# Kernel optimization log

Measured on AMD Instinct MI355X. Metric: run time of the kernel, lower is better.

## Reference

```python
import jax, jax.numpy as jnp
import numpy as np

EMBED_DIM = 1024
NUM_HEADS = 16
HEAD_DIM = EMBED_DIM // NUM_HEADS
SCALE = HEAD_DIM ** -0.5


def setup_inputs() -> dict:
    key = jax.random.key(0)
    k_x, k_qkv, k_proj = jax.random.split(key, 3)
    x = jax.random.normal(k_x, (2, 2048, EMBED_DIM), dtype=jnp.float32)
    # nn.Linear weights: [out_features, in_features]
    w_qkv = jax.random.normal(k_qkv, (3 * EMBED_DIM, EMBED_DIM), dtype=jnp.float32) * (EMBED_DIM ** -0.5)
    w_proj = jax.random.normal(k_proj, (EMBED_DIM, EMBED_DIM), dtype=jnp.float32) * (EMBED_DIM ** -0.5)
    return {"x": x, "w_qkv": w_qkv, "w_proj": w_proj}


def reference(x, w_qkv, w_proj):
    B, N, C = x.shape
    # fused QKV projection: [B,N,3C]
    qkv = jnp.einsum('bnc,oc->bno', x, w_qkv)
    qkv = qkv.reshape(B, N, 3, NUM_HEADS, HEAD_DIM)
    q, k, v = jnp.moveaxis(qkv, 2, 0)  # each [B, N, H, D]
    q = q.transpose(0, 2, 1, 3)  # [B, H, N, D]
    k = k.transpose(0, 2, 1, 3)
    v = v.transpose(0, 2, 1, 3)
    # scaled dot-product attention (eval mode: dropout_p=0, non-causal)
    scores = jnp.einsum('bhqd,bhkd->bhqk', q, k) * SCALE
    attn = jax.nn.softmax(scores, axis=-1)
    out = jnp.einsum('bhqk,bhkd->bhqd', attn, v)  # [B, H, N, D]
    out = out.transpose(0, 2, 1, 3).reshape(B, N, C)
    return jnp.einsum('bnc,oc->bno', out, w_proj)
```

## Files before the change

### kernel.cpp

```cpp
#include <hip/hip_runtime.h>
#include <hip/hip_bf16.h>

typedef __bf16 bf16;
typedef __bf16 bf16x8 __attribute__((ext_vector_type(8)));
typedef __bf16 bf16x4 __attribute__((ext_vector_type(4)));
typedef _Float16 f16;
typedef _Float16 f16x4 __attribute__((ext_vector_type(4)));
typedef float f32x4 __attribute__((ext_vector_type(4)));

#define MFMA16(a, b, c)    __builtin_amdgcn_mfma_f32_16x16x32_bf16(a, b, c, 0, 0, 0)
#define MFMA16F16(a, b, c) __builtin_amdgcn_mfma_f32_16x16x16f16(a, b, c, 0, 0, 0)

__device__ __forceinline__ void gll(const void* g, void* l) {
    __builtin_amdgcn_global_load_lds(
        (const __attribute__((address_space(1))) unsigned int*)g,
        (__attribute__((address_space(3))) unsigned int*)l, 16, 0, 0);
}

__global__ void cvt_all(const float* __restrict__ x, const float* __restrict__ wq,
                        const float* __restrict__ wp, bf16* __restrict__ xb,
                        bf16* __restrict__ wqb, bf16* __restrict__ wpb) {
    int i = blockIdx.x * 256 + threadIdx.x;
    const float4* s; bf16* d; int j;
    if (i < 1048576)                { s = (const float4*)x;  d = xb;  j = i; }
    else if (i < 1048576 + 786432)  { s = (const float4*)wq; d = wqb; j = i - 1048576; }
    else                            { s = (const float4*)wp; d = wpb; j = i - 1835008; }
    float4 f = s[j];
    bf16x4 o; o[0] = (bf16)f.x; o[1] = (bf16)f.y; o[2] = (bf16)f.z; o[3] = (bf16)f.w;
    ((bf16x4*)d)[j] = o;
}

#define QSCALE 0.18033688f

__global__ __launch_bounds__(256, 3) void gemm_qkv(
    const bf16* __restrict__ A, const bf16* __restrict__ Bm,
    bf16* __restrict__ qo, bf16* __restrict__ ko, f16* __restrict__ vo)
{
    __shared__ bf16 As[2][128 * 32];
    __shared__ bf16 Bs[2][128 * 32];
    const int tid = threadIdx.x;
    const int wave = tid >> 6, lane = tid & 63;
    const int lrow = lane & 15, quad = lane >> 4;
    const int wm = (wave >> 1) * 64, wn = (wave & 1) * 64;
    const int srow = tid >> 2;
    const int scol = ((tid & 3) ^ (srow & 3)) * 8;
    const int fsw = (quad ^ (lrow & 3)) * 8;

    const bf16* Ap = A + (long)(blockIdx.x * 128 + srow) * 1024 + scol;
    const bf16* Bp = Bm + (long)(blockIdx.y * 128 + srow) * 1024 + scol;

    f32x4 acc[4][4] = {};
    const int gm0 = blockIdx.x * 128 + wm;
    const int go0 = blockIdx.y * 128 + wn;

    gll(Ap, &As[0][tid * 8]);  gll(Ap + 64 * 1024, &As[0][2048 + tid * 8]);
    gll(Bp, &Bs[0][tid * 8]);  gll(Bp + 64 * 1024, &Bs[0][2048 + tid * 8]);

    if (blockIdx.y < 16) {
        for (int i = 0; i < 32; i++) {
            const int cur = i & 1;
            __syncthreads();
            if (i < 31) {
                const int k0 = (i + 1) * 32;
                gll(Ap + k0, &As[cur ^ 1][tid * 8]);
                gll(Ap + 64 * 1024 + k0, &As[cur ^ 1][2048 + tid * 8]);
                gll(Bp + k0, &Bs[cur ^ 1][tid * 8]);
                gll(Bp + 64 * 1024 + k0, &Bs[cur ^ 1][2048 + tid * 8]);
            }
            bf16x8 af[4], bfr[4];
#pragma unroll
            for (int ii = 0; ii < 4; ii++) af[ii] = *(const bf16x8*)&As[cur][(wm + ii * 16 + lrow) * 32 + fsw];
#pragma unroll
            for (int j = 0; j < 4; j++) bfr[j] = *(const bf16x8*)&Bs[cur][(wn + j * 16 + lrow) * 32 + fsw];
#pragma unroll
            for (int ii = 0; ii < 4; ii++)
#pragma unroll
                for (int j = 0; j < 4; j++)
                    acc[ii][j] = MFMA16(bfr[j], af[ii], acc[ii][j]);
        }
        const bool isQ = blockIdx.y < 8;
        bf16* dst = isQ ? qo : ko;
        const float sc = isQ ? QSCALE : 1.0f;
#pragma unroll
        for (int i = 0; i < 4; i++) {
            int gm = gm0 + i * 16 + lrow;
            int b = gm >> 11, n = gm & 2047;
#pragma unroll
            for (int j = 0; j < 4; j++) {
                int ob = go0 + j * 16 + quad * 4;
                int rem = ob & 1023;
                int h = rem >> 6, d0 = rem & 63;
                bf16x4 pk;
#pragma unroll
                for (int r = 0; r < 4; r++) pk[r] = (bf16)(acc[i][j][r] * sc);
                *(bf16x4*)&dst[((long)(b * 16 + h) * 2048 + n) * 64 + d0] = pk;
            }
        }
    } else {
        for (int i = 0; i < 32; i++) {
            const int cur = i & 1;
            __syncthreads();
            if (i < 31) {
                const int k0 = (i + 1) * 32;
                gll(Ap + k0, &As[cur ^ 1][tid * 8]);
                gll(Ap + 64 * 1024 + k0, &As[cur ^ 1][2048 + tid * 8]);
                gll(Bp + k0, &Bs[cur ^ 1][tid * 8]);
                gll(Bp + 64 * 1024 + k0, &Bs[cur ^ 1][2048 + tid * 8]);
            }
            bf16x8 af[4], bfr[4];
#pragma unroll
            for (int ii = 0; ii < 4; ii++) af[ii] = *(const bf16x8*)&As[cur][(wm + ii * 16 + lrow) * 32 + fsw];
#pragma unroll
            for (int j = 0; j < 4; j++) bfr[j] = *(const bf16x8*)&Bs[cur][(wn + j * 16 + lrow) * 32 + fsw];
#pragma unroll
            for (int ii = 0; ii < 4; ii++)
#pragma unroll
                for (int j = 0; j < 4; j++)
                    acc[ii][j] = MFMA16(af[ii], bfr[j], acc[ii][j]);
        }
#pragma unroll
        for (int i = 0; i < 4; i++) {
            int gmb = gm0 + i * 16 + quad * 4;
            int b = gmb >> 11, nb = gmb & 2047;
#pragma unroll
            for (int j = 0; j < 4; j++) {
                int o = go0 + j * 16 + lrow;
                int rem = o & 1023;
                int h = rem >> 6, d = rem & 63;
                f16x4 pk;
#pragma unroll
                for (int r = 0; r < 4; r++) pk[r] = (f16)acc[i][j][r];
                *(f16x4*)&vo[(((long)(b * 16 + h)) * 64 + d) * 2048 + nb] = pk;
            }
        }
    }
}

__global__ __launch_bounds__(256, 2) void attn_kernel(
    const bf16* __restrict__ q, const bf16* __restrict__ k,
    const f16* __restrict__ vt, bf16* __restrict__ o)
{
    __shared__ __align__(16) char smem[35328];
    bf16* KsB = (bf16*)smem;

    const int tid = threadIdx.x, wave = tid >> 6, lane = tid & 63;
    const int lrow = lane & 15, quad = lane >> 4;
    const int qh = wave & 1, kh = wave >> 1;
    const int bh = blockIdx.x & 31, qt = blockIdx.x >> 5;
    const bf16* Qp = q + ((long)bh * 2048 + qt * 128 + qh * 64) * 64;
    const bf16* Kp = k + (long)bh * 2048 * 64;
    const f16*  Vp = vt + (long)bh * 64 * 2048;

    const int sr = tid >> 3;
    const int scc = ((tid & 7) ^ (sr & 7)) * 8;

    bf16x8 qf[4][2];
#pragma unroll
    for (int t = 0; t < 4; t++)
#pragma unroll
        for (int ks = 0; ks < 2; ks++)
            qf[t][ks] = *(const bf16x8*)&Qp[(t * 16 + lrow) * 64 + ks * 32 + quad * 8];
    asm volatile("s_waitcnt vmcnt(0)" ::: "memory");

#pragma unroll
    for (int b = 0; b < 2; b++) {
        gll(Kp + b * 4096 + sr * 64 + scc,        KsB + b * 4096 + tid * 8);
        gll(Kp + b * 4096 + (sr + 32) * 64 + scc, KsB + b * 4096 + 2048 + tid * 8);
    }

    f32x4 oacc[4][4] = {};
    float lsum[4] = {0.f, 0.f, 0.f, 0.f};

    for (int kv = 0; kv < 32; kv++) {
        asm volatile("s_waitcnt vmcnt(2)" ::: "memory");
        __builtin_amdgcn_s_barrier();
        asm volatile("" ::: "memory");

        f16x4 vfr[2][4];
#pragma unroll
        for (int n = 0; n < 2; n++)
#pragma unroll
            for (int jd = 0; jd < 4; jd++)
                vfr[n][jd] = *(const f16x4*)&Vp[(long)(jd * 16 + lrow) * 2048 +
                                                kv * 64 + kh * 32 + n * 16 + quad * 4];

        if (kv < 30) {
            bf16* kd = KsB + ((kv + 2) & 3) * 4096;
            gll(Kp + (kv + 2) * 4096 + sr * 64 + scc,        kd + tid * 8);
            gll(Kp + (kv + 2) * 4096 + (sr + 32) * 64 + scc, kd + 2048 + tid * 8);
        }

        const bf16* Kc = KsB + (kv & 3) * 4096;

        bf16x8 kf[2][2];
#pragma unroll
        for (int ks = 0; ks < 2; ks++)
#pragma unroll
            for (int n = 0; n < 2; n++)
                kf[ks][n] = *(const bf16x8*)&Kc[(kh * 32 + n * 16 + lrow) * 64 +
                                                (((ks * 4 + quad) ^ (lrow & 7)) * 8)];
        f32x4 sacc[4][2];
#pragma unroll
        for (int t = 0; t < 4; t++)
#pragma unroll
            for (int n = 0; n < 2; n++) sacc[t][n] = f32x4{-8.f, -8.f, -8.f, -8.f};
        __builtin_amdgcn_s_setprio(1);
#pragma unroll
        for (int ks = 0; ks < 2; ks++)
#pragma unroll
            for (int t = 0; t < 4; t++)
#pragma unroll
                for (int n = 0; n < 2; n++)
                    sacc[t][n] = MFMA16(kf[ks][n], qf[t][ks], sacc[t][n]);
        __builtin_amdgcn_s_setprio(0);

        f16x4 pa[4][2];
#pragma unroll
        for (int t = 0; t < 4; t++)
#pragma unroll
            for (int n = 0; n < 2; n++)
#pragma unroll
                for (int r = 0; r < 4; r++) {
                    float p = __builtin_exp2f(sacc[t][n][r]);
                    lsum[t] += p;
                    pa[t][n][r] = (f16)p;
                }

        __builtin_amdgcn_s_setprio(1);
#pragma unroll
        for (int jd = 0; jd < 4; jd++)
#pragma unroll
            for (int t = 0; t < 4; t++)
#pragma unroll
                for (int n = 0; n < 2; n++)
                    oacc[t][jd] = MFMA16F16(pa[t][n], vfr[n][jd], oacc[t][jd]);
        __builtin_amdgcn_s_setprio(0);
    }

#pragma unroll
    for (int t = 0; t < 4; t++) {
        lsum[t] += __shfl_xor(lsum[t], 16, 64);
        lsum[t] += __shfl_xor(lsum[t], 32, 64);
    }

    __syncthreads();
    float* Pt  = (float*)smem;
    float* lsL = (float*)(smem + 34816);
    float* Pr  = Pt + qh * (64 * 68);
    if (kh == 1) {
#pragma unroll
        for (int t = 0; t < 4; t++)
#pragma unroll
            for (int jd = 0; jd < 4; jd++)
                *(f32x4*)&Pr[lane * 68 + (t * 4 + jd) * 4] = oacc[t][jd];
        if (quad == 0)
#pragma unroll
            for (int t = 0; t < 4; t++) lsL[qh * 64 + t * 16 + lrow] = lsum[t];
    }
    __syncthreads();
    if (kh == 0) {
#pragma unroll
        for (int t = 0; t < 4; t++)
#pragma unroll
            for (int jd = 0; jd < 4; jd++)
                oacc[t][jd] += *(const f32x4*)&Pr[lane * 68 + (t * 4 + jd) * 4];
#pragma unroll
        for (int t = 0; t < 4; t++) lsum[t] += lsL[qh * 64 + t * 16 + lrow];

        bf16* Tw = (bf16*)Pr;
        const int b = bh >> 4, h = bh & 15;
#pragma unroll
        for (int t = 0; t < 4; t++) {
            float linv = 1.0f / lsum[t];
#pragma unroll
            for (int r = 0; r < 4; r++) {
                float lr = __shfl(linv, quad * 4 + r, 64);
#pragma unroll
                for (int jd = 0; jd < 4; jd++)
                    Tw[(t * 16 + quad * 4 + r) * 72 + jd * 16 + lrow] = (bf16)(oacc[t][jd][r] * lr);
            }
        }
        const int rr = lane >> 3, cc = (lane & 7) * 8;
#pragma unroll
        for (int p = 0; p < 8; p++) {
            bf16x8 val = *(const bf16x8*)&Tw[(rr + p * 8) * 72 + cc];
            int n = qt * 128 + qh * 64 + rr + p * 8;
            *(bf16x8*)&o[((long)(b * 2048 + n)) * 1024 + h * 64 + cc] = val;
        }
    }
}

__global__ __launch_bounds__(256, 2) void gemm_proj(
    const bf16* __restrict__ A, const bf16* __restrict__ Bm, float* __restrict__ out)
{
    __shared__ bf16 As[2][128 * 32];
    __shared__ bf16 Bs[2][64 * 32];
    const int tid = threadIdx.x;
    const int wave = tid >> 6, lane = tid & 63;
    const int lrow = lane & 15, quad = lane >> 4;
    const int wm = (wave >> 1) * 64, wn = (wave & 1) * 32;
    const int srow = tid >> 2;
    const int scol = ((tid & 3) ^ (srow & 3)) * 8;
    const int fsw = (quad ^ (lrow & 3)) * 8;

    const bf16* Ap = A + (long)(blockIdx.x * 128 + srow) * 1024 + scol;
    const bf16* Bp = Bm + (long)(blockIdx.y * 64 + srow) * 1024 + scol;

    f32x4 acc[4][2] = {};

    gll(Ap, &As[0][tid * 8]);  gll(Ap + 64 * 1024, &As[0][2048 + tid * 8]);
    gll(Bp, &Bs[0][tid * 8]);

    for (int i = 0; i < 32; i++) {
        const int cur = i & 1;
        __syncthreads();
        if (i < 31) {
            const int k0 = (i + 1) * 32;
            gll(Ap + k0, &As[cur ^ 1][tid * 8]);
            gll(Ap + 64 * 1024 + k0, &As[cur ^ 1][2048 + tid * 8]);
            gll(Bp + k0, &Bs[cur ^ 1][tid * 8]);
        }
        bf16x8 af[4], bfr[2];
#pragma unroll
        for (int ii = 0; ii < 4; ii++) af[ii] = *(const bf16x8*)&As[cur][(wm + ii * 16 + lrow) * 32 + fsw];
#pragma unroll
        for (int j = 0; j < 2; j++) bfr[j] = *(const bf16x8*)&Bs[cur][(wn + j * 16 + lrow) * 32 + fsw];
#pragma unroll
        for (int ii = 0; ii < 4; ii++)
#pragma unroll
            for (int j = 0; j < 2; j++)
                acc[ii][j] = MFMA16(bfr[j], af[ii], acc[ii][j]);
    }

    const int gm0 = blockIdx.x * 128 + wm;
    const int go0 = blockIdx.y * 64 + wn;
#pragma unroll
    for (int i = 0; i < 4; i++) {
        int gm = gm0 + i * 16 + lrow;
#pragma unroll
        for (int j = 0; j < 2; j++) {
            int ob = go0 + j * 16 + quad * 4;
            *(f32x4*)&out[(long)gm * 1024 + ob] = acc[i][j];
        }
    }
}

extern "C" void kernel_launch(void* const* d_in, const int* in_sizes, int n_in,
                              void* d_out, int out_size, void* d_ws, size_t ws_size,
                              hipStream_t stream) {
    const float* x      = (const float*)d_in[0];
    const float* w_qkv  = (const float*)d_in[1];
    const float* w_proj = (const float*)d_in[2];
    float* out = (float*)d_out;

    bf16* ws = (bf16*)d_ws;
    bf16* xb     = ws;
    bf16* wqkvb  = xb + 4096 * 1024;
    bf16* wprojb = wqkvb + 3072 * 1024;
    bf16* qb     = wprojb + 1024 * 1024;
    bf16* kb     = qb + 2 * 16 * 2048 * 64;
    f16*  vb     = (f16*)(kb + 2 * 16 * 2048 * 64);
    bf16* ob     = (bf16*)(vb + 2 * 16 * 2048 * 64);

    cvt_all<<<8192, 256, 0, stream>>>(x, w_qkv, w_proj, xb, wqkvb, wprojb);
    gemm_qkv<<<dim3(32, 24), 256, 0, stream>>>(xb, wqkvb, qb, kb, vb);
    attn_kernel<<<512, 256, 0, stream>>>(qb, kb, vb, ob);
    gemm_proj<<<dim3(32, 16), 256, 0, stream>>>(ob, wprojb, out);
}
```

Before: 205.0 us.

## Stage V tiles through LDS and halve attention query tile per block

The attention kernel now loads V into a swizzled LDS buffer with async global-to-LDS copies, alongside K, in a three-slot ring instead of reading V fragments straight from global memory. Each block handles 64 query rows instead of 128, so the grid doubles to 1024 blocks, and the launch bound asks for 3 blocks per CU. The aim is to avoid strided uncoalesced global V reads and to improve occupancy and latency hiding. In exchange, each K/V tile is reused by fewer query rows, which raises total K/V traffic from L2, and the larger LDS footprint may limit how many blocks fit per CU.

```diff
diff --git a/kernel.cpp b/kernel.cpp
--- a/kernel.cpp
+++ b/kernel.cpp
@@ -136,61 +136,65 @@
     }
 }
 
-__global__ __launch_bounds__(256, 2) void attn_kernel(
+__global__ __launch_bounds__(256, 3) void attn_kernel(
     const bf16* __restrict__ q, const bf16* __restrict__ k,
     const f16* __restrict__ vt, bf16* __restrict__ o)
 {
-    __shared__ __align__(16) char smem[35328];
+    __shared__ __align__(16) char smem[49152];
     bf16* KsB = (bf16*)smem;
+    f16*  VsB = (f16*)(smem + 24576);
 
     const int tid = threadIdx.x, wave = tid >> 6, lane = tid & 63;
     const int lrow = lane & 15, quad = lane >> 4;
-    const int qh = wave & 1, kh = wave >> 1;
+    const int qg = wave & 1, kh = wave >> 1;
     const int bh = blockIdx.x & 31, qt = blockIdx.x >> 5;
-    const bf16* Qp = q + ((long)bh * 2048 + qt * 128 + qh * 64) * 64;
+    const bf16* Qp = q + ((long)bh * 2048 + qt * 64 + qg * 32) * 64;
     const bf16* Kp = k + (long)bh * 2048 * 64;
     const f16*  Vp = vt + (long)bh * 64 * 2048;
 
     const int sr = tid >> 3;
     const int scc = ((tid & 7) ^ (sr & 7)) * 8;
 
-    bf16x8 qf[4][2];
-#pragma unroll
-    for (int t = 0; t < 4; t++)
+    bf16x8 qf[2][2];
+#pragma unroll
+    for (int t = 0; t < 2; t++)
 #pragma unroll
         for (int ks = 0; ks < 2; ks++)
             qf[t][ks] = *(const bf16x8*)&Qp[(t * 16 + lrow) * 64 + ks * 32 + quad * 8];
     asm volatile("s_waitcnt vmcnt(0)" ::: "memory");
 
 #pragma unroll
-    for (int b = 0; b < 2; b++) {
-        gll(Kp + b * 4096 + sr * 64 + scc,        KsB + b * 4096 + tid * 8);
-        gll(Kp + b * 4096 + (sr + 32) * 64 + scc, KsB + b * 4096 + 2048 + tid * 8);
-    }
-
-    f32x4 oacc[4][4] = {};
-    float lsum[4] = {0.f, 0.f, 0.f, 0.f};
-
+    for (int b = 0; b < 2; b++)
+#pragma unroll
+        for (int p = 0; p < 2; p++) {
+            gll(Kp + b * 4096 + (sr + 32 * p) * 64 + scc,        KsB + b * 4096 + p * 2048 + tid * 8);
+            gll(Vp + b * 64 + (long)(sr + 32 * p) * 2048 + scc,  VsB + b * 4096 + p * 2048 + tid * 8);
+        }
+
+    f32x4 oacc[2][4] = {};
+    float lsum[2] = {0.f, 0.f};
+
+    int cur = 0, nx = 2;
     for (int kv = 0; kv < 32; kv++) {
-        asm volatile("s_waitcnt vmcnt(2)" ::: "memory");
+        if (kv < 31) { asm volatile("s_waitcnt vmcnt(4)" ::: "memory"); }
+        else         { asm volatile("s_waitcnt vmcnt(0)" ::: "memory"); }
         __builtin_amdgcn_s_barrier();
         asm volatile("" ::: "memory");
 
-        f16x4 vfr[2][4];
-#pragma unroll
-        for (int n = 0; n < 2; n++)
-#pragma unroll
-            for (int jd = 0; jd < 4; jd++)
-                vfr[n][jd] = *(const f16x4*)&Vp[(long)(jd * 16 + lrow) * 2048 +
-                                                kv * 64 + kh * 32 + n * 16 + quad * 4];
-
         if (kv < 30) {
-            bf16* kd = KsB + ((kv + 2) & 3) * 4096;
-            gll(Kp + (kv + 2) * 4096 + sr * 64 + scc,        kd + tid * 8);
-            gll(Kp + (kv + 2) * 4096 + (sr + 32) * 64 + scc, kd + 2048 + tid * 8);
-        }
-
-        const bf16* Kc = KsB + (kv & 3) * 4096;
+            const bf16* Kn = Kp + (kv + 2) * 4096;
+            const f16*  Vn = Vp + (kv + 2) * 64;
+            bf16* kd = KsB + nx * 4096;
+            f16*  vd = VsB + nx * 4096;
+#pragma unroll
+            for (int p = 0; p < 2; p++) {
+                gll(Kn + (sr + 32 * p) * 64 + scc,         kd + p * 2048 + tid * 8);
+                gll(Vn + (long)(sr + 32 * p) * 2048 + scc, vd + p * 2048 + tid * 8);
+            }
+        }
+
+        const bf16* Kc = KsB + cur * 4096;
+        const f16*  Vc = VsB + cur * 4096;
 
         bf16x8 kf[2][2];
 #pragma unroll
@@ -199,24 +203,24 @@
             for (int n = 0; n < 2; n++)
                 kf[ks][n] = *(const bf16x8*)&Kc[(kh * 32 + n * 16 + lrow) * 64 +
                                                 (((ks * 4 + quad) ^ (lrow & 7)) * 8)];
-        f32x4 sacc[4][2];
-#pragma unroll
-        for (int t = 0; t < 4; t++)
+        f32x4 sacc[2][2];
+#pragma unroll
+        for (int t = 0; t < 2; t++)
 #pragma unroll
             for (int n = 0; n < 2; n++) sacc[t][n] = f32x4{-8.f, -8.f, -8.f, -8.f};
         __builtin_amdgcn_s_setprio(1);
 #pragma unroll
         for (int ks = 0; ks < 2; ks++)
 #pragma unroll
-            for (int t = 0; t < 4; t++)
+            for (int t = 0; t < 2; t++)
 #pragma unroll
                 for (int n = 0; n < 2; n++)
                     sacc[t][n] = MFMA16(kf[ks][n], qf[t][ks], sacc[t][n]);
         __builtin_amdgcn_s_setprio(0);
 
-        f16x4 pa[4][2];
-#pragma unroll
-        for (int t = 0; t < 4; t++)
+        f16x4 pa[2][2];
+#pragma unroll
+        for (int t = 0; t < 2; t++)
 #pragma unroll
             for (int n = 0; n < 2; n++)
 #pragma unroll
@@ -228,49 +232,60 @@
 
         __builtin_amdgcn_s_setprio(1);
 #pragma unroll
-        for (int jd = 0; jd < 4; jd++)
-#pragma unroll
-            for (int t = 0; t < 4; t++)
+        for (int jd = 0; jd < 4; jd++) {
+            f16x4 vf[2];
+#pragma unroll
+            for (int n = 0; n < 2; n++) {
+                int cs = kh * 4 + n * 2 + (quad >> 1);
+                vf[n] = *(const f16x4*)&Vc[(jd * 16 + lrow) * 64 +
+                                           ((cs ^ (lrow & 7)) * 8) + (quad & 1) * 4];
+            }
+#pragma unroll
+            for (int t = 0; t < 2; t++)
 #pragma unroll
                 for (int n = 0; n < 2; n++)
-                    oacc[t][jd] = MFMA16F16(pa[t][n], vfr[n][jd], oacc[t][jd]);
+                    oacc[t][jd] = MFMA16F16(pa[t][n], vf[n], oacc[t][jd]);
+        }
         __builtin_amdgcn_s_setprio(0);
-    }
-
-#pragma unroll
-    for (int t = 0; t < 4; t++) {
+
+        cur = (cur == 2) ? 0 : cur + 1;
+        nx  = (nx == 2) ? 0 : nx + 1;
+    }
+
+#pragma unroll
+    for (int t = 0; t < 2; t++) {
         lsum[t] += __shfl_xor(lsum[t], 16, 64);
         lsum[t] += __shfl_xor(lsum[t], 32, 64);
     }
 
     __syncthreads();
     float* Pt  = (float*)smem;
-    float* lsL = (float*)(smem + 34816);
-    float* Pr  = Pt + qh * (64 * 68);
+    float* lsL = (float*)(smem + 18432);
+    float* Pr  = Pt + qg * (64 * 36);
     if (kh == 1) {
 #pragma unroll
-        for (int t = 0; t < 4; t++)
+        for (int t = 0; t < 2; t++)
 #pragma unroll
             for (int jd = 0; jd < 4; jd++)
-                *(f32x4*)&Pr[lane * 68 + (t * 4 + jd) * 4] = oacc[t][jd];
+                *(f32x4*)&Pr[lane * 36 + (t * 4 + jd) * 4] = oacc[t][jd];
         if (quad == 0)
 #pragma unroll
-            for (int t = 0; t < 4; t++) lsL[qh * 64 + t * 16 + lrow] = lsum[t];
+            for (int t = 0; t < 2; t++) lsL[qg * 32 + t * 16 + lrow] = lsum[t];
     }
     __syncthreads();
     if (kh == 0) {
 #pragma unroll
-        for (int t = 0; t < 4; t++)
+        for (int t = 0; t < 2; t++)
 #pragma unroll
             for (int jd = 0; jd < 4; jd++)
-                oacc[t][jd] += *(const f32x4*)&Pr[lane * 68 + (t * 4 + jd) * 4];
-#pragma unroll
-        for (int t = 0; t < 4; t++) lsum[t] += lsL[qh * 64 + t * 16 + lrow];
+                oacc[t][jd] += *(const f32x4*)&Pr[lane * 36 + (t * 4 + jd) * 4];
+#pragma unroll
+        for (int t = 0; t < 2; t++) lsum[t] += lsL[qg * 32 + t * 16 + lrow];
 
         bf16* Tw = (bf16*)Pr;
         const int b = bh >> 4, h = bh & 15;
 #pragma unroll
-        for (int t = 0; t < 4; t++) {
+        for (int t = 0; t < 2; t++) {
             float linv = 1.0f / lsum[t];
 #pragma unroll
             for (int r = 0; r < 4; r++) {
@@ -282,9 +297,9 @@
         }
         const int rr = lane >> 3, cc = (lane & 7) * 8;
 #pragma unroll
-        for (int p = 0; p < 8; p++) {
+        for (int p = 0; p < 4; p++) {
             bf16x8 val = *(const bf16x8*)&Tw[(rr + p * 8) * 72 + cc];
-            int n = qt * 128 + qh * 64 + rr + p * 8;
+            int n = qt * 64 + qg * 32 + rr + p * 8;
             *(bf16x8*)&o[((long)(b * 2048 + n)) * 1024 + h * 64 + cc] = val;
         }
     }
@@ -364,6 +379,6 @@
 
     cvt_all<<<8192, 256, 0, stream>>>(x, w_qkv, w_proj, xb, wqkvb, wprojb);
     gemm_qkv<<<dim3(32, 24), 256, 0, stream>>>(xb, wqkvb, qb, kb, vb);
-    attn_kernel<<<512, 256, 0, stream>>>(qb, kb, vb, ob);
+    attn_kernel<<<1024, 256, 0, stream>>>(qb, kb, vb, ob);
     gemm_proj<<<dim3(32, 16), 256, 0, stream>>>(ob, wprojb, out);
 }
```

After: 193.1 us. -5.8%, faster.

## Store Q/K/V in MFMA-fragment-native tiles and load attention operands directly from global

Applied to the files above, without the earlier changes.

The QKV GEMM epilogue now writes Q, K and V in a pre-swizzled tiled layout matching each lane's MFMA fragment. The attention kernel can then read K and V fragments with contiguous 16-byte per-lane global loads instead of staging K through LDS behind barriers. A two-tile register double-buffer replaces the LDS ring buffer to overlap loads with compute. This removes LDS traffic and per-iteration barriers, but each wave now loads K/V separately from global/L2 and register pressure rises. The initial __syncthreads before the epilogue is also dropped, which appears safe because K is no longer staged in shared memory.

```diff
diff --git a/kernel.cpp b/kernel.cpp
--- a/kernel.cpp
+++ b/kernel.cpp
@@ -6,6 +6,7 @@
 typedef __bf16 bf16x4 __attribute__((ext_vector_type(4)));
 typedef _Float16 f16;
 typedef _Float16 f16x4 __attribute__((ext_vector_type(4)));
+typedef _Float16 f16x8 __attribute__((ext_vector_type(8)));
 typedef float f32x4 __attribute__((ext_vector_type(4)));
 
 #define MFMA16(a, b, c)    __builtin_amdgcn_mfma_f32_16x16x32_bf16(a, b, c, 0, 0, 0)
@@ -31,6 +32,7 @@
 }
 
 #define QSCALE 0.18033688f
+
 
 __global__ __launch_bounds__(256, 3) void gemm_qkv(
     const bf16* __restrict__ A, const bf16* __restrict__ Bm,
@@ -81,21 +83,20 @@
         const bool isQ = blockIdx.y < 8;
         bf16* dst = isQ ? qo : ko;
         const float sc = isQ ? QSCALE : 1.0f;
-#pragma unroll
-        for (int i = 0; i < 4; i++) {
-            int gm = gm0 + i * 16 + lrow;
-            int b = gm >> 11, n = gm & 2047;
+        const int b = gm0 >> 11;
+        const int h = (go0 & 1023) >> 6;
+        const long tbase = ((long)(b * 16 + h) * 32 + ((gm0 >> 6) & 31)) * 4096;
+#pragma unroll
+        for (int i = 0; i < 4; i++)
 #pragma unroll
             for (int j = 0; j < 4; j++) {
-                int ob = go0 + j * 16 + quad * 4;
-                int rem = ob & 1023;
-                int h = rem >> 6, d0 = rem & 63;
                 bf16x4 pk;
 #pragma unroll
                 for (int r = 0; r < 4; r++) pk[r] = (bf16)(acc[i][j][r] * sc);
-                *(bf16x4*)&dst[((long)(b * 16 + h) * 2048 + n) * 64 + d0] = pk;
-            }
-        }
+                long Aoff = tbase + (i * 2 + (j >> 1)) * 512
+                          + ((j & 1) * 2 + (quad >> 1)) * 128 + lrow * 8 + (quad & 1) * 4;
+                *(bf16x4*)&dst[Aoff] = pk;
+            }
     } else {
         for (int i = 0; i < 32; i++) {
             const int cur = i & 1;
@@ -118,123 +119,113 @@
                 for (int j = 0; j < 4; j++)
                     acc[ii][j] = MFMA16(af[ii], bfr[j], acc[ii][j]);
         }
-#pragma unroll
-        for (int i = 0; i < 4; i++) {
-            int gmb = gm0 + i * 16 + quad * 4;
-            int b = gmb >> 11, nb = gmb & 2047;
+        const int b = gm0 >> 11;
+        const int h = (go0 & 1023) >> 6;
+        const long tbase = ((long)(b * 16 + h) * 32 + ((gm0 >> 6) & 31)) * 4096;
+#pragma unroll
+        for (int i = 0; i < 4; i++)
 #pragma unroll
             for (int j = 0; j < 4; j++) {
-                int o = go0 + j * 16 + lrow;
-                int rem = o & 1023;
-                int h = rem >> 6, d = rem & 63;
                 f16x4 pk;
 #pragma unroll
                 for (int r = 0; r < 4; r++) pk[r] = (f16)acc[i][j][r];
-                *(f16x4*)&vo[(((long)(b * 16 + h)) * 64 + d) * 2048 + nb] = pk;
-            }
-        }
-    }
+                long Aoff = tbase + (i >> 1) * 2048 + j * 512
+                          + (quad * 16 + lrow) * 8 + (i & 1) * 4;
+                *(f16x4*)&vo[Aoff] = pk;
+            }
+    }
+}
+
+__device__ __forceinline__ void load_tile(const bf16* Kt, const f16* Vt, int kh, int lane,
+                                          bf16x8 kf[2][2], f16x8 vf[4]) {
+#pragma unroll
+    for (int ks = 0; ks < 2; ks++)
+#pragma unroll
+        for (int n = 0; n < 2; n++)
+            kf[ks][n] = *(const bf16x8*)&Kt[((kh * 2 + n) * 2 + ks) * 512 + lane * 8];
+#pragma unroll
+    for (int jd = 0; jd < 4; jd++)
+        vf[jd] = *(const f16x8*)&Vt[jd * 512 + lane * 8];
+}
+
+__device__ __forceinline__ void compute_tile(const bf16x8 kf[2][2], const f16x8 vf[4],
+                                             const bf16x8 qf[4][2],
+                                             f32x4 oacc[4][4], float lsum[4]) {
+    f32x4 sacc[4][2];
+#pragma unroll
+    for (int t = 0; t < 4; t++)
+#pragma unroll
+        for (int n = 0; n < 2; n++) sacc[t][n] = f32x4{-8.f, -8.f, -8.f, -8.f};
+    __builtin_amdgcn_s_setprio(1);
+#pragma unroll
+    for (int ks = 0; ks < 2; ks++)
+#pragma unroll
+        for (int t = 0; t < 4; t++)
+#pragma unroll
+            for (int n = 0; n < 2; n++)
+                sacc[t][n] = MFMA16(kf[ks][n], qf[t][ks], sacc[t][n]);
+    __builtin_amdgcn_s_setprio(0);
+
+    f16x4 pa[4][2];
+#pragma unroll
+    for (int t = 0; t < 4; t++)
+#pragma unroll
+        for (int n = 0; n < 2; n++)
+#pragma unroll
+            for (int r = 0; r < 4; r++) {
+                float p = __builtin_exp2f(sacc[t][n][r]);
+                lsum[t] += p;
+                pa[t][n][r] = (f16)p;
+            }
+
+    __builtin_amdgcn_s_setprio(1);
+#pragma unroll
+    for (int jd = 0; jd < 4; jd++) {
+        f16x4 lo = __builtin_shufflevector(vf[jd], vf[jd], 0, 1, 2, 3);
+        f16x4 hi = __builtin_shufflevector(vf[jd], vf[jd], 4, 5, 6, 7);
+#pragma unroll
+        for (int t = 0; t < 4; t++) {
+            oacc[t][jd] = MFMA16F16(pa[t][0], lo, oacc[t][jd]);
+            oacc[t][jd] = MFMA16F16(pa[t][1], hi, oacc[t][jd]);
+        }
+    }
+    __builtin_amdgcn_s_setprio(0);
 }
 
 __global__ __launch_bounds__(256, 2) void attn_kernel(
-    const bf16* __restrict__ q, const bf16* __restrict__ k,
-    const f16* __restrict__ vt, bf16* __restrict__ o)
+    const bf16* __restrict__ qp, const bf16* __restrict__ kp,
+    const f16* __restrict__ vp, bf16* __restrict__ o)
 {
     __shared__ __align__(16) char smem[35328];
-    bf16* KsB = (bf16*)smem;
 
     const int tid = threadIdx.x, wave = tid >> 6, lane = tid & 63;
     const int lrow = lane & 15, quad = lane >> 4;
     const int qh = wave & 1, kh = wave >> 1;
     const int bh = blockIdx.x & 31, qt = blockIdx.x >> 5;
-    const bf16* Qp = q + ((long)bh * 2048 + qt * 128 + qh * 64) * 64;
-    const bf16* Kp = k + (long)bh * 2048 * 64;
-    const f16*  Vp = vt + (long)bh * 64 * 2048;
-
-    const int sr = tid >> 3;
-    const int scc = ((tid & 7) ^ (sr & 7)) * 8;
+    const bf16* Qb = qp + ((long)bh * 32 + qt * 2 + qh) * 4096;
+    const bf16* Kb = kp + (long)bh * 32 * 4096;
+    const f16*  Vb = vp + (long)bh * 32 * 4096 + kh * 2048;
 
     bf16x8 qf[4][2];
 #pragma unroll
     for (int t = 0; t < 4; t++)
 #pragma unroll
         for (int ks = 0; ks < 2; ks++)
-            qf[t][ks] = *(const bf16x8*)&Qp[(t * 16 + lrow) * 64 + ks * 32 + quad * 8];
-    asm volatile("s_waitcnt vmcnt(0)" ::: "memory");
-
-#pragma unroll
-    for (int b = 0; b < 2; b++) {
-        gll(Kp + b * 4096 + sr * 64 + scc,        KsB + b * 4096 + tid * 8);
-        gll(Kp + b * 4096 + (sr + 32) * 64 + scc, KsB + b * 4096 + 2048 + tid * 8);
-    }
+            qf[t][ks] = *(const bf16x8*)&Qb[(t * 2 + ks) * 512 + lane * 8];
 
     f32x4 oacc[4][4] = {};
     float lsum[4] = {0.f, 0.f, 0.f, 0.f};
 
-    for (int kv = 0; kv < 32; kv++) {
-        asm volatile("s_waitcnt vmcnt(2)" ::: "memory");
-        __builtin_amdgcn_s_barrier();
-        asm volatile("" ::: "memory");
-
-        f16x4 vfr[2][4];
-#pragma unroll
-        for (int n = 0; n < 2; n++)
-#pragma unroll
-            for (int jd = 0; jd < 4; jd++)
-                vfr[n][jd] = *(const f16x4*)&Vp[(long)(jd * 16 + lrow) * 2048 +
-                                                kv * 64 + kh * 32 + n * 16 + quad * 4];
-
-        if (kv < 30) {
-            bf16* kd = KsB + ((kv + 2) & 3) * 4096;
-            gll(Kp + (kv + 2) * 4096 + sr * 64 + scc,        kd + tid * 8);
-            gll(Kp + (kv + 2) * 4096 + (sr + 32) * 64 + scc, kd + 2048 + tid * 8);
-        }
-
-        const bf16* Kc = KsB + (kv & 3) * 4096;
-
-        bf16x8 kf[2][2];
-#pragma unroll
-        for (int ks = 0; ks < 2; ks++)
-#pragma unroll
-            for (int n = 0; n < 2; n++)
-                kf[ks][n] = *(const bf16x8*)&Kc[(kh * 32 + n * 16 + lrow) * 64 +
-                                                (((ks * 4 + quad) ^ (lrow & 7)) * 8)];
-        f32x4 sacc[4][2];
-#pragma unroll
-        for (int t = 0; t < 4; t++)
-#pragma unroll
-            for (int n = 0; n < 2; n++) sacc[t][n] = f32x4{-8.f, -8.f, -8.f, -8.f};
-        __builtin_amdgcn_s_setprio(1);
-#pragma unroll
-        for (int ks = 0; ks < 2; ks++)
-#pragma unroll
-            for (int t = 0; t < 4; t++)
-#pragma unroll
-                for (int n = 0; n < 2; n++)
-                    sacc[t][n] = MFMA16(kf[ks][n], qf[t][ks], sacc[t][n]);
-        __builtin_amdgcn_s_setprio(0);
-
-        f16x4 pa[4][2];
-#pragma unroll
-        for (int t = 0; t < 4; t++)
-#pragma unroll
-            for (int n = 0; n < 2; n++)
-#pragma unroll
-                for (int r = 0; r < 4; r++) {
-                    float p = __builtin_exp2f(sacc[t][n][r]);
-                    lsum[t] += p;
-                    pa[t][n][r] = (f16)p;
-                }
-
-        __builtin_amdgcn_s_setprio(1);
-#pragma unroll
-        for (int jd = 0; jd < 4; jd++)
-#pragma unroll
-            for (int t = 0; t < 4; t++)
-#pragma unroll
-                for (int n = 0; n < 2; n++)
-                    oacc[t][jd] = MFMA16F16(pa[t][n], vfr[n][jd], oacc[t][jd]);
-        __builtin_amdgcn_s_setprio(0);
+    bf16x8 kA[2][2], kB[2][2];
+    f16x8  vA[4], vB[4];
+    load_tile(Kb, Vb, kh, lane, kA, vA);
+
+    for (int kv = 0; kv < 32; kv += 2) {
+        load_tile(Kb + (kv + 1) * 4096, Vb + (long)(kv + 1) * 4096, kh, lane, kB, vB);
+        compute_tile(kA, vA, qf, oacc, lsum);
+        if (kv < 30)
+            load_tile(Kb + (kv + 2) * 4096, Vb + (long)(kv + 2) * 4096, kh, lane, kA, vA);
+        compute_tile(kB, vB, qf, oacc, lsum);
     }
 
 #pragma unroll
@@ -243,7 +234,6 @@
         lsum[t] += __shfl_xor(lsum[t], 32, 64);
     }
 
-    __syncthreads();
     float* Pt  = (float*)smem;
     float* lsL = (float*)(smem + 34816);
     float* Pr  = Pt + qh * (64 * 68);
```

Result: faster. 182.1 us (-11.2%).
